# Kernel optimization log

Measured on AMD Instinct MI355X. Metric: run time of the kernel, lower is better.

## Reference

```python
import jax, jax.numpy as jnp
import numpy as np

HIDDEN = 1024
HEADS = 16
HEAD_DIM = HIDDEN // HEADS

def setup_inputs() -> dict:
    key = jax.random.key(0)
    k1, k2, k3 = jax.random.split(key, 3)
    scale = 1.0 / np.sqrt(HIDDEN)
    return {
        "x": jax.random.normal(k1, (2, 2048, HIDDEN), dtype=jnp.float32),
        "w_qkv": jax.random.normal(k2, (HIDDEN, 3 * HIDDEN), dtype=jnp.float32) * scale,
        "b_qkv": jnp.zeros((3 * HIDDEN,), dtype=jnp.float32),
        "w_out": jax.random.normal(k3, (HIDDEN, HIDDEN), dtype=jnp.float32) * scale,
        "b_out": jnp.zeros((HIDDEN,), dtype=jnp.float32),
    }

def reference(x, w_qkv, b_qkv, w_out, b_out):
    B, S, H = x.shape
    qkv = x @ w_qkv + b_qkv                              # (B,S,3H)
    qkv = qkv.reshape(B, S, 3, HEADS, HEAD_DIM)
    qkv = jnp.transpose(qkv, (2, 0, 3, 1, 4))            # (3,B,nh,S,hd)
    q, k, v = qkv[0], qkv[1], qkv[2]
    scores = jnp.einsum("bhqd,bhkd->bhqk", q, k) / np.sqrt(HEAD_DIM)
    causal = jnp.triu(jnp.ones((S, S), dtype=bool), k=1)  # True above diagonal
    scores = jnp.where(causal, -jnp.inf, scores)
    attn = jax.nn.softmax(scores, axis=-1)               # dropout: eval mode (identity)
    out = jnp.einsum("bhqk,bhkd->bhqd", attn, v)
    out = jnp.transpose(out, (0, 2, 1, 3)).reshape(B, S, H)
    return out @ w_out + b_out
```

## Files before the change

kernel.cpp:

```cpp
#include <hip/hip_runtime.h>
#include <hip/hip_bf16.h>

typedef short short8 __attribute__((ext_vector_type(8)));
typedef short short4v __attribute__((ext_vector_type(4)));
typedef unsigned int uint4v __attribute__((ext_vector_type(4)));
typedef float f32x4 __attribute__((ext_vector_type(4)));

typedef const __attribute__((address_space(1))) unsigned int* gas_ptr;
typedef __attribute__((address_space(3))) unsigned int* las_ptr;
#define ASYNC16(g, l) __builtin_amdgcn_global_load_lds((gas_ptr)(g), (las_ptr)(l), 16, 0, 0)

__device__ __forceinline__ unsigned short f2bf(float f) {
    unsigned int u = __builtin_bit_cast(unsigned int, f);
    u += 0x7fff + ((u >> 16) & 1);
    return (unsigned short)(u >> 16);
}
__device__ __forceinline__ float bf2f(unsigned short s) {
    unsigned int u = (unsigned int)s << 16;
    return __builtin_bit_cast(float, u);
}
__device__ __forceinline__ unsigned int pkbf_trunc(float lo, float hi) {
    return __builtin_amdgcn_perm(__builtin_bit_cast(unsigned int, hi),
                                 __builtin_bit_cast(unsigned int, lo), 0x07060302u);
}

__device__ __forceinline__ void transpose_tile(
    const float* __restrict__ w, unsigned short* __restrict__ wt,
    int K, int N, int k0, int n0, unsigned short* tile)
{
    for (int i = threadIdx.x; i < 64 * 64; i += 256) {
        int r = i >> 6, c = i & 63;
        tile[r * 65 + c] = f2bf(w[(size_t)(k0 + r) * N + n0 + c]);
    }
    __syncthreads();
    for (int i = threadIdx.x; i < 64 * 64; i += 256) {
        int r = i >> 6, c = i & 63;
        wt[(size_t)(n0 + r) * K + k0 + c] = tile[c * 65 + r];
    }
}

__global__ __launch_bounds__(256) void prep(
    const float* __restrict__ x, const float* __restrict__ w_qkv,
    const float* __restrict__ w_out,
    unsigned short* __restrict__ x_b, unsigned short* __restrict__ wqkv_t,
    unsigned short* __restrict__ wout_t)
{
    __shared__ unsigned short tile[64 * 65];
    int bid = blockIdx.x;
    if (bid < 4096) {
        int i = (bid * 256 + threadIdx.x) * 4;
        float4 v = *(const float4*)(x + i);
        ushort4 o;
        o.x = f2bf(v.x); o.y = f2bf(v.y); o.z = f2bf(v.z); o.w = f2bf(v.w);
        *(ushort4*)(x_b + i) = o;
    } else if (bid < 4096 + 768) {
        int t = bid - 4096;
        transpose_tile(w_qkv, wqkv_t, 1024, 3072, (t / 48) * 64, (t % 48) * 64, tile);
    } else {
        int t = bid - 4864;
        transpose_tile(w_out, wout_t, 1024, 1024, (t >> 4) * 64, (t & 15) * 64, tile);
    }
}


template<bool OUT_BF16, bool QKV>
__global__ __launch_bounds__(256, 3) void gemm_bt(
    const unsigned short* __restrict__ A,
    const unsigned short* __restrict__ Bt,
    const float* __restrict__ bias,
    void* __restrict__ C,
    unsigned short* __restrict__ vTp,
    int M, int N, int K)
{
    __shared__ __align__(16) unsigned short As[128 * 32];
    __shared__ __align__(16) unsigned short Bs[128 * 32];
    const int tid = threadIdx.x;
    const int lane = tid & 63;
    const int wave = tid >> 6;
    const int wr = wave >> 1, wc = wave & 1;
    const int m0 = blockIdx.x * 128, n0 = blockIdx.y * 128;
    const int fr = lane & 15, fq = lane >> 4;

    f32x4 acc[4][4] = {};

    const int grow = lane >> 2;
    const int gcol = (lane & 3) * 8;
    const unsigned short* Ag = A  + (size_t)(m0 + wave * 32 + grow) * K + gcol;
    const unsigned short* Bg = Bt + (size_t)(n0 + wave * 32 + grow) * K + gcol;
    unsigned short* AsW0 = As + (wave * 32) * 32;
    unsigned short* AsW1 = As + (wave * 32 + 16) * 32;
    unsigned short* BsW0 = Bs + (wave * 32) * 32;
    unsigned short* BsW1 = Bs + (wave * 32 + 16) * 32;

    for (int k0 = 0; k0 < K; k0 += 32) {
        __syncthreads();
        ASYNC16(Ag + k0,          AsW0);
        ASYNC16(Ag + 16 * K + k0, AsW1);
        ASYNC16(Bg + k0,          BsW0);
        ASYNC16(Bg + 16 * K + k0, BsW1);
        __syncthreads();

        short8 af[4], bfr[4];
#pragma unroll
        for (int i = 0; i < 4; i++)
            af[i] = *(const short8*)(As + (wr * 64 + i * 16 + fr) * 32 + fq * 8);
#pragma unroll
        for (int j = 0; j < 4; j++)
            bfr[j] = *(const short8*)(Bs + (wc * 64 + j * 16 + fr) * 32 + fq * 8);
#pragma unroll
        for (int i = 0; i < 4; i++)
#pragma unroll
            for (int j = 0; j < 4; j++)
                acc[i][j] = __builtin_amdgcn_mfma_f32_16x16x32_bf16(af[i], bfr[j], acc[i][j], 0, 0, 0);
    }

#pragma unroll
    for (int i = 0; i < 4; i++)
#pragma unroll
        for (int j = 0; j < 4; j++) {
            int col = n0 + wc * 64 + j * 16 + fr;
            float bv = bias[col];
            if (QKV && col >= 2048) {
                int hh = (col - 2048) >> 6, d = col & 63;
#pragma unroll
                for (int r = 0; r < 4; r++) {
                    int row = m0 + wr * 64 + i * 16 + fq * 4 + r;
                    int bb = row >> 11, s = row & 2047;
                    vTp[((size_t)(bb * 16 + hh) * 64 + d) * 2048 + s] = f2bf(acc[i][j][r] + bv);
                }
            } else {
                const int cstride = QKV ? 2048 : N;
#pragma unroll
                for (int r = 0; r < 4; r++) {
                    int row = m0 + wr * 64 + i * 16 + fq * 4 + r;
                    float v = acc[i][j][r] + bv;
                    if (OUT_BF16)
                        ((unsigned short*)C)[(size_t)row * cstride + col] = f2bf(v);
                    else
                        ((float*)C)[(size_t)row * cstride + col] = v;
                }
            }
        }
}


template<int RG0>
__device__ __forceinline__ void attn_step(
    const unsigned short* __restrict__ Ks0, const unsigned short* __restrict__ Ks1,
    const unsigned short* __restrict__ Vs0, const unsigned short* __restrict__ Vs1,
    const short8 (&qf)[4][2], const short8 ones,
    f32x4 (&o_acc)[4][4], f32x4 (&l_acc)[4],
    int j0, int fr, int fq,
    const int (&qrow0)[4], bool diagA, bool diagB)
{
    short8 kf[4][2];
#pragma unroll
    for (int t = 0; t < 4; t++) {
        kf[t][0] = *(const short8*)(Ks0 + (t * 16 + fr) * 32 + fq * 8);
        kf[t][1] = *(const short8*)(Ks1 + (t * 16 + fr) * 32 + fq * 8);
    }

    short8 pf[4][2];
#pragma unroll
    for (int rg = RG0; rg < 4; rg++) {
        f32x4 s[4];
#pragma unroll
        for (int t = 0; t < 4; t++) {
            s[t] = (f32x4){0.f, 0.f, 0.f, 0.f};
            s[t] = __builtin_amdgcn_mfma_f32_16x16x32_bf16(kf[t][0], qf[rg][0], s[t], 0, 0, 0);
            s[t] = __builtin_amdgcn_mfma_f32_16x16x32_bf16(kf[t][1], qf[rg][1], s[t], 0, 0, 0);
        }
        const bool diag = (rg < 2) ? diagA : diagB;
        unsigned int pk[4][2];
        if (diag) {
            const int qq = qrow0[rg] + fr;
#pragma unroll
            for (int t = 0; t < 4; t++) {
                const int keyb = j0 + t * 16 + fq * 4;
                float p[4];
#pragma unroll
                for (int r = 0; r < 4; r++) {
                    float v = __expf(s[t][r] * 0.125f - 8.0f);
                    if (keyb + r > qq) v = 0.f;
                    p[r] = v;
                }
                pk[t][0] = pkbf_trunc(p[0], p[1]);
                pk[t][1] = pkbf_trunc(p[2], p[3]);
            }
        } else {
#pragma unroll
            for (int t = 0; t < 4; t++) {
                float p[4];
#pragma unroll
                for (int r = 0; r < 4; r++)
                    p[r] = __expf(s[t][r] * 0.125f - 8.0f);
                pk[t][0] = pkbf_trunc(p[0], p[1]);
                pk[t][1] = pkbf_trunc(p[2], p[3]);
            }
        }
        pf[rg][0] = __builtin_bit_cast(short8, (uint4v){pk[0][0], pk[0][1], pk[1][0], pk[1][1]});
        pf[rg][1] = __builtin_bit_cast(short8, (uint4v){pk[2][0], pk[2][1], pk[3][0], pk[3][1]});
    }

#pragma unroll
    for (int ks = 0; ks < 2; ks++) {
        const unsigned short* Vsb = ks ? Vs1 : Vs0;
#pragma unroll
        for (int t = 0; t < 4; t++) {
            short4v vlo = *(const short4v*)(Vsb + (t * 16 + fr) * 32 + fq * 4);
            short4v vhi = *(const short4v*)(Vsb + (t * 16 + fr) * 32 + 16 + fq * 4);
            short8 vf = (short8){vlo[0], vlo[1], vlo[2], vlo[3], vhi[0], vhi[1], vhi[2], vhi[3]};
#pragma unroll
            for (int rg = RG0; rg < 4; rg++)
                o_acc[rg][t] = __builtin_amdgcn_mfma_f32_16x16x32_bf16(vf, pf[rg][ks], o_acc[rg][t], 0, 0, 0);
        }
#pragma unroll
        for (int rg = RG0; rg < 4; rg++)
            l_acc[rg] = __builtin_amdgcn_mfma_f32_16x16x32_bf16(ones, pf[rg][ks], l_acc[rg], 0, 0, 0);
    }
}

__global__ __launch_bounds__(128, 2) void flash_attn(
    const unsigned short* __restrict__ qkv,
    const unsigned short* __restrict__ vT,
    unsigned short* __restrict__ Opart,
    float* __restrict__ lpart)
{
    const int gid = blockIdx.x;
    const int bh = gid & 31;
    const int sl = gid >> 5;
    const int p  = sl & 15;
    const int g  = sl >> 4;
    const int h = bh & 15, b = bh >> 4;
    const int tid = threadIdx.x, wave = tid >> 6, lane = tid & 63;
    const int fr = lane & 15, fq = lane >> 4;
    const size_t RS = 2048;

    const unsigned short* Qb = qkv + (size_t)b * 2048 * RS + h * 64;
    const unsigned short* Kb = Qb + 1024;
    const unsigned short* Vt = vT + (size_t)(b * 16 + h) * 64 * 2048;

    __shared__ __align__(16) unsigned short Ks[2][64 * 32];
    __shared__ __align__(16) unsigned short Vs[2][64 * 32];

    short8 qf[4][2];
    int qrow0[4];
#pragma unroll
    for (int rg = 0; rg < 4; rg++) {
        int qt = (rg < 2) ? p : (31 - p);
        qrow0[rg] = qt * 64 + wave * 32 + (rg & 1) * 16;
        const unsigned short* qrow = Qb + (size_t)(qrow0[rg] + fr) * RS;
        qf[rg][0] = *(const short8*)(qrow + fq * 8);
        qf[rg][1] = *(const short8*)(qrow + 32 + fq * 8);
    }
    short8 ones;
#pragma unroll
    for (int e = 0; e < 8; e++) ones[e] = (short)0x3F80;

    f32x4 o_acc[4][4] = {};
    f32x4 l_acc[4] = {};

    const int grow = lane >> 2;
    const int gcol = (lane & 3) * 8;
    const unsigned short* Kg = Kb + (size_t)(wave * 32 + grow) * RS + gcol;
    const unsigned short* Vg = Vt + (size_t)(wave * 32 + grow) * 2048 + gcol;
    unsigned short* KsW00 = Ks[0] + (wave * 32) * 32;
    unsigned short* KsW01 = Ks[0] + (wave * 32 + 16) * 32;
    unsigned short* KsW10 = Ks[1] + (wave * 32) * 32;
    unsigned short* KsW11 = Ks[1] + (wave * 32 + 16) * 32;
    unsigned short* VsW00 = Vs[0] + (wave * 32) * 32;
    unsigned short* VsW01 = Vs[0] + (wave * 32 + 16) * 32;
    unsigned short* VsW10 = Vs[1] + (wave * 32) * 32;
    unsigned short* VsW11 = Vs[1] + (wave * 32 + 16) * 32;

    const int njt = 32 - p;
    int lo = (g == 0) ? 0 : njt;
    int hi = njt;
    {
        int cum = 0;
        bool flo = (g == 0), fhi = false;
        for (int j = 0; j < njt; j++) {
            if (!flo && cum >= 44 * g)        { lo = j; flo = true; }
            if (!fhi && cum >= 44 * (g + 1))  { hi = j; fhi = true; }
            cum += (j <= p) ? 8 : 4;
        }
    }

    for (int jt = lo; jt < hi; jt++) {
        const int j0 = jt * 64;
        __syncthreads();
        ASYNC16(Kg + (size_t)j0 * RS,               KsW00);
        ASYNC16(Kg + (size_t)(j0 + 16) * RS,        KsW01);
        ASYNC16(Kg + (size_t)j0 * RS + 32,          KsW10);
        ASYNC16(Kg + (size_t)(j0 + 16) * RS + 32,   KsW11);
        ASYNC16(Vg + j0,               VsW00);
        ASYNC16(Vg + 16 * 2048 + j0,   VsW01);
        ASYNC16(Vg + j0 + 32,          VsW10);
        ASYNC16(Vg + 16 * 2048 + j0 + 32, VsW11);
        __syncthreads();

        bool diagA = (jt == p), diagB = (jt == 31 - p);
        if (jt <= p)
            attn_step<0>(Ks[0], Ks[1], Vs[0], Vs[1], qf, ones,
                         o_acc, l_acc, j0, fr, fq, qrow0, diagA, diagB);
        else
            attn_step<2>(Ks[0], Ks[1], Vs[0], Vs[1], qf, ones,
                         o_acc, l_acc, j0, fr, fq, qrow0, diagA, diagB);
    }

    unsigned short* Og = Opart + (size_t)g * 4096 * 1024;
    float* lg = lpart + (size_t)g * 4096 * 16;
#pragma unroll
    for (int rg = 0; rg < 4; rg++) {
        const size_t rowbase = (size_t)(b * 2048 + qrow0[rg] + fr) * 1024 + h * 64;
#pragma unroll
        for (int t = 0; t < 4; t++) {
            ushort4 o;
            o.x = f2bf(o_acc[rg][t][0]); o.y = f2bf(o_acc[rg][t][1]);
            o.z = f2bf(o_acc[rg][t][2]); o.w = f2bf(o_acc[rg][t][3]);
            *(ushort4*)(Og + rowbase + t * 16 + fq * 4) = o;
        }
        if (fq == 0)
            lg[(size_t)(b * 2048 + qrow0[rg] + fr) * 16 + h] = l_acc[rg][0];
    }
}

__global__ __launch_bounds__(256) void reduce_attn(
    const unsigned short* __restrict__ Opart, const float* __restrict__ lpart,
    unsigned short* __restrict__ out)
{
    const size_t OP = (size_t)4096 * 1024, LP = (size_t)4096 * 16;
    int i = (blockIdx.x * 256 + threadIdx.x) * 8;
    int row = i >> 10, h = (i & 1023) >> 6;
    float lsum = lpart[row * 16 + h] + lpart[LP + row * 16 + h] + lpart[2 * LP + row * 16 + h];
    float inv = 1.0f / lsum;
    float acc[8];
#pragma unroll
    for (int e = 0; e < 8; e++) acc[e] = 0.f;
#pragma unroll
    for (int gpart = 0; gpart < 3; gpart++) {
        ushort4 a0 = *(const ushort4*)(Opart + gpart * OP + i);
        ushort4 a1 = *(const ushort4*)(Opart + gpart * OP + i + 4);
        acc[0] += bf2f(a0.x); acc[1] += bf2f(a0.y); acc[2] += bf2f(a0.z); acc[3] += bf2f(a0.w);
        acc[4] += bf2f(a1.x); acc[5] += bf2f(a1.y); acc[6] += bf2f(a1.z); acc[7] += bf2f(a1.w);
    }
    ushort4 o0, o1;
    o0.x = f2bf(acc[0] * inv); o0.y = f2bf(acc[1] * inv);
    o0.z = f2bf(acc[2] * inv); o0.w = f2bf(acc[3] * inv);
    o1.x = f2bf(acc[4] * inv); o1.y = f2bf(acc[5] * inv);
    o1.z = f2bf(acc[6] * inv); o1.w = f2bf(acc[7] * inv);
    *(ushort4*)(out + i) = o0;
    *(ushort4*)(out + i + 4) = o1;
}

extern "C" void kernel_launch(void* const* d_in, const int* in_sizes, int n_in,
                              void* d_out, int out_size, void* d_ws, size_t ws_size,
                              hipStream_t stream) {
    const float* x      = (const float*)d_in[0];
    const float* w_qkv  = (const float*)d_in[1];
    const float* b_qkv  = (const float*)d_in[2];
    const float* w_out  = (const float*)d_in[3];
    const float* b_out  = (const float*)d_in[4];
    float* out = (float*)d_out;

    char* ws = (char*)d_ws;
    const size_t MB = 1024 * 1024;
    unsigned short* qkv    = (unsigned short*)(ws);
    unsigned short* vT     = (unsigned short*)(ws + 16 * MB);
    unsigned short* wout_t = (unsigned short*)(ws + 24 * MB);
    unsigned short* attn   = (unsigned short*)(ws + 26 * MB);
    float*          lpart  = (float*)         (ws + 34 * MB);
    unsigned short* x_b    = (unsigned short*)(ws + 36 * MB);
    unsigned short* wqkv_t = (unsigned short*)(ws + 44 * MB);
    unsigned short* Opart  = (unsigned short*)(ws + 36 * MB);

    prep<<<5120, 256, 0, stream>>>(x, w_qkv, w_out, x_b, wqkv_t, wout_t);
    gemm_bt<true, true ><<<dim3(32, 24), 256, 0, stream>>>(x_b,  wqkv_t, b_qkv, qkv, vT, 4096, 3072, 1024);
    flash_attn<<<1536, 128, 0, stream>>>(qkv, vT, Opart, lpart);
    reduce_attn<<<2048, 256, 0, stream>>>(Opart, lpart, attn);
    gemm_bt<false, false><<<dim3(32, 8),  256, 0, stream>>>(attn, wout_t, b_out, out, nullptr, 4096, 1024, 1024);
}
```

Measured before the change: 212.0 us.

## Rework flash attention to 4 waves per block with 2-way KV split

Flash attention blocks now run four waves of 16 query rows each instead of two waves of 32. The key range is split into two partitions with a simple fixed midpoint instead of three partitions balanced by a cost loop, and the reduce kernel sums two partials instead of three. The V tile is now written to LDS with a per-row rotation and read back with the matching offset, to cut bank conflicts on the V fragment loads. Each wave holds fewer accumulators, which should allow more resident waves, but the fixed split may balance work unevenly across blocks.

```diff
diff --git a/kernel.cpp b/kernel.cpp
--- a/kernel.cpp
+++ b/kernel.cpp
@@ -148,10 +148,10 @@
 __device__ __forceinline__ void attn_step(
     const unsigned short* __restrict__ Ks0, const unsigned short* __restrict__ Ks1,
     const unsigned short* __restrict__ Vs0, const unsigned short* __restrict__ Vs1,
-    const short8 (&qf)[4][2], const short8 ones,
-    f32x4 (&o_acc)[4][4], f32x4 (&l_acc)[4],
+    const short8 (&qf)[2][2], const short8 ones,
+    f32x4 (&o_acc)[2][4], f32x4 (&l_acc)[2],
     int j0, int fr, int fq,
-    const int (&qrow0)[4], bool diagA, bool diagB)
+    const int (&qrow0)[2], bool diagA, bool diagB)
 {
     short8 kf[4][2];
 #pragma unroll
@@ -160,9 +160,9 @@
         kf[t][1] = *(const short8*)(Ks1 + (t * 16 + fr) * 32 + fq * 8);
     }
 
-    short8 pf[4][2];
-#pragma unroll
-    for (int rg = RG0; rg < 4; rg++) {
+    short8 pf[2][2];
+#pragma unroll
+    for (int rg = RG0; rg < 2; rg++) {
         f32x4 s[4];
 #pragma unroll
         for (int t = 0; t < 4; t++) {
@@ -170,7 +170,7 @@
             s[t] = __builtin_amdgcn_mfma_f32_16x16x32_bf16(kf[t][0], qf[rg][0], s[t], 0, 0, 0);
             s[t] = __builtin_amdgcn_mfma_f32_16x16x32_bf16(kf[t][1], qf[rg][1], s[t], 0, 0, 0);
         }
-        const bool diag = (rg < 2) ? diagA : diagB;
+        const bool diag = rg ? diagB : diagA;
         unsigned int pk[4][2];
         if (diag) {
             const int qq = qrow0[rg] + fr;
@@ -202,25 +202,28 @@
         pf[rg][1] = __builtin_bit_cast(short8, (uint4v){pk[2][0], pk[2][1], pk[3][0], pk[3][1]});
     }
 
+    const int rot = (fr & 3) * 8;
+    const int eo_lo = (fq * 4 - rot) & 31;
+    const int eo_hi = (fq * 4 + 16 - rot) & 31;
 #pragma unroll
     for (int ks = 0; ks < 2; ks++) {
         const unsigned short* Vsb = ks ? Vs1 : Vs0;
 #pragma unroll
         for (int t = 0; t < 4; t++) {
-            short4v vlo = *(const short4v*)(Vsb + (t * 16 + fr) * 32 + fq * 4);
-            short4v vhi = *(const short4v*)(Vsb + (t * 16 + fr) * 32 + 16 + fq * 4);
+            short4v vlo = *(const short4v*)(Vsb + (t * 16 + fr) * 32 + eo_lo);
+            short4v vhi = *(const short4v*)(Vsb + (t * 16 + fr) * 32 + eo_hi);
             short8 vf = (short8){vlo[0], vlo[1], vlo[2], vlo[3], vhi[0], vhi[1], vhi[2], vhi[3]};
 #pragma unroll
-            for (int rg = RG0; rg < 4; rg++)
+            for (int rg = RG0; rg < 2; rg++)
                 o_acc[rg][t] = __builtin_amdgcn_mfma_f32_16x16x32_bf16(vf, pf[rg][ks], o_acc[rg][t], 0, 0, 0);
         }
 #pragma unroll
-        for (int rg = RG0; rg < 4; rg++)
+        for (int rg = RG0; rg < 2; rg++)
             l_acc[rg] = __builtin_amdgcn_mfma_f32_16x16x32_bf16(ones, pf[rg][ks], l_acc[rg], 0, 0, 0);
     }
 }
 
-__global__ __launch_bounds__(128, 2) void flash_attn(
+__global__ __launch_bounds__(256, 3) void flash_attn(
     const unsigned short* __restrict__ qkv,
     const unsigned short* __restrict__ vT,
     unsigned short* __restrict__ Opart,
@@ -243,12 +246,12 @@
     __shared__ __align__(16) unsigned short Ks[2][64 * 32];
     __shared__ __align__(16) unsigned short Vs[2][64 * 32];
 
-    short8 qf[4][2];
-    int qrow0[4];
-#pragma unroll
-    for (int rg = 0; rg < 4; rg++) {
-        int qt = (rg < 2) ? p : (31 - p);
-        qrow0[rg] = qt * 64 + wave * 32 + (rg & 1) * 16;
+    short8 qf[2][2];
+    int qrow0[2];
+#pragma unroll
+    for (int rg = 0; rg < 2; rg++) {
+        int qt = rg ? (31 - p) : p;
+        qrow0[rg] = qt * 64 + wave * 16;
         const unsigned short* qrow = Qb + (size_t)(qrow0[rg] + fr) * RS;
         qf[rg][0] = *(const short8*)(qrow + fq * 8);
         qf[rg][1] = *(const short8*)(qrow + 32 + fq * 8);
@@ -257,46 +260,31 @@
 #pragma unroll
     for (int e = 0; e < 8; e++) ones[e] = (short)0x3F80;
 
-    f32x4 o_acc[4][4] = {};
-    f32x4 l_acc[4] = {};
+    f32x4 o_acc[2][4] = {};
+    f32x4 l_acc[2] = {};
 
     const int grow = lane >> 2;
     const int gcol = (lane & 3) * 8;
-    const unsigned short* Kg = Kb + (size_t)(wave * 32 + grow) * RS + gcol;
-    const unsigned short* Vg = Vt + (size_t)(wave * 32 + grow) * 2048 + gcol;
-    unsigned short* KsW00 = Ks[0] + (wave * 32) * 32;
-    unsigned short* KsW01 = Ks[0] + (wave * 32 + 16) * 32;
-    unsigned short* KsW10 = Ks[1] + (wave * 32) * 32;
-    unsigned short* KsW11 = Ks[1] + (wave * 32 + 16) * 32;
-    unsigned short* VsW00 = Vs[0] + (wave * 32) * 32;
-    unsigned short* VsW01 = Vs[0] + (wave * 32 + 16) * 32;
-    unsigned short* VsW10 = Vs[1] + (wave * 32) * 32;
-    unsigned short* VsW11 = Vs[1] + (wave * 32 + 16) * 32;
-
-    const int njt = 32 - p;
-    int lo = (g == 0) ? 0 : njt;
-    int hi = njt;
-    {
-        int cum = 0;
-        bool flo = (g == 0), fhi = false;
-        for (int j = 0; j < njt; j++) {
-            if (!flo && cum >= 44 * g)        { lo = j; flo = true; }
-            if (!fhi && cum >= 44 * (g + 1))  { hi = j; fhi = true; }
-            cum += (j <= p) ? 8 : 4;
-        }
-    }
+    const int vrot = (grow & 3) * 8;
+    const int vcol = (gcol + vrot) & 31;
+    const unsigned short* Kg = Kb + (size_t)(wave * 16 + grow) * RS + gcol;
+    const unsigned short* Vg = Vt + (size_t)(wave * 16 + grow) * 2048 + vcol;
+    unsigned short* KsW0 = Ks[0] + (wave * 16) * 32;
+    unsigned short* KsW1 = Ks[1] + (wave * 16) * 32;
+    unsigned short* VsW0 = Vs[0] + (wave * 16) * 32;
+    unsigned short* VsW1 = Vs[1] + (wave * 16) * 32;
+
+    const int mid = (p >= 8) ? 8 : (16 - p);
+    const int lo = g ? mid : 0;
+    const int hi = g ? (32 - p) : mid;
 
     for (int jt = lo; jt < hi; jt++) {
         const int j0 = jt * 64;
         __syncthreads();
-        ASYNC16(Kg + (size_t)j0 * RS,               KsW00);
-        ASYNC16(Kg + (size_t)(j0 + 16) * RS,        KsW01);
-        ASYNC16(Kg + (size_t)j0 * RS + 32,          KsW10);
-        ASYNC16(Kg + (size_t)(j0 + 16) * RS + 32,   KsW11);
-        ASYNC16(Vg + j0,               VsW00);
-        ASYNC16(Vg + 16 * 2048 + j0,   VsW01);
-        ASYNC16(Vg + j0 + 32,          VsW10);
-        ASYNC16(Vg + 16 * 2048 + j0 + 32, VsW11);
+        ASYNC16(Kg + (size_t)j0 * RS,      KsW0);
+        ASYNC16(Kg + (size_t)j0 * RS + 32, KsW1);
+        ASYNC16(Vg + j0,      VsW0);
+        ASYNC16(Vg + j0 + 32, VsW1);
         __syncthreads();
 
         bool diagA = (jt == p), diagB = (jt == 31 - p);
@@ -304,14 +292,14 @@
             attn_step<0>(Ks[0], Ks[1], Vs[0], Vs[1], qf, ones,
                          o_acc, l_acc, j0, fr, fq, qrow0, diagA, diagB);
         else
-            attn_step<2>(Ks[0], Ks[1], Vs[0], Vs[1], qf, ones,
+            attn_step<1>(Ks[0], Ks[1], Vs[0], Vs[1], qf, ones,
                          o_acc, l_acc, j0, fr, fq, qrow0, diagA, diagB);
     }
 
     unsigned short* Og = Opart + (size_t)g * 4096 * 1024;
     float* lg = lpart + (size_t)g * 4096 * 16;
 #pragma unroll
-    for (int rg = 0; rg < 4; rg++) {
+    for (int rg = 0; rg < 2; rg++) {
         const size_t rowbase = (size_t)(b * 2048 + qrow0[rg] + fr) * 1024 + h * 64;
 #pragma unroll
         for (int t = 0; t < 4; t++) {
@@ -332,23 +320,21 @@
     const size_t OP = (size_t)4096 * 1024, LP = (size_t)4096 * 16;
     int i = (blockIdx.x * 256 + threadIdx.x) * 8;
     int row = i >> 10, h = (i & 1023) >> 6;
-    float lsum = lpart[row * 16 + h] + lpart[LP + row * 16 + h] + lpart[2 * LP + row * 16 + h];
+    float lsum = lpart[row * 16 + h] + lpart[LP + row * 16 + h];
     float inv = 1.0f / lsum;
-    float acc[8];
-#pragma unroll
-    for (int e = 0; e < 8; e++) acc[e] = 0.f;
-#pragma unroll
-    for (int gpart = 0; gpart < 3; gpart++) {
-        ushort4 a0 = *(const ushort4*)(Opart + gpart * OP + i);
-        ushort4 a1 = *(const ushort4*)(Opart + gpart * OP + i + 4);
-        acc[0] += bf2f(a0.x); acc[1] += bf2f(a0.y); acc[2] += bf2f(a0.z); acc[3] += bf2f(a0.w);
-        acc[4] += bf2f(a1.x); acc[5] += bf2f(a1.y); acc[6] += bf2f(a1.z); acc[7] += bf2f(a1.w);
-    }
+    ushort4 a0 = *(const ushort4*)(Opart + i);
+    ushort4 a1 = *(const ushort4*)(Opart + i + 4);
+    ushort4 b0 = *(const ushort4*)(Opart + OP + i);
+    ushort4 b1 = *(const ushort4*)(Opart + OP + i + 4);
     ushort4 o0, o1;
-    o0.x = f2bf(acc[0] * inv); o0.y = f2bf(acc[1] * inv);
-    o0.z = f2bf(acc[2] * inv); o0.w = f2bf(acc[3] * inv);
-    o1.x = f2bf(acc[4] * inv); o1.y = f2bf(acc[5] * inv);
-    o1.z = f2bf(acc[6] * inv); o1.w = f2bf(acc[7] * inv);
+    o0.x = f2bf((bf2f(a0.x) + bf2f(b0.x)) * inv);
+    o0.y = f2bf((bf2f(a0.y) + bf2f(b0.y)) * inv);
+    o0.z = f2bf((bf2f(a0.z) + bf2f(b0.z)) * inv);
+    o0.w = f2bf((bf2f(a0.w) + bf2f(b0.w)) * inv);
+    o1.x = f2bf((bf2f(a1.x) + bf2f(b1.x)) * inv);
+    o1.y = f2bf((bf2f(a1.y) + bf2f(b1.y)) * inv);
+    o1.z = f2bf((bf2f(a1.z) + bf2f(b1.z)) * inv);
+    o1.w = f2bf((bf2f(a1.w) + bf2f(b1.w)) * inv);
     *(ushort4*)(out + i) = o0;
     *(ushort4*)(out + i + 4) = o1;
 }
@@ -376,7 +362,7 @@
 
     prep<<<5120, 256, 0, stream>>>(x, w_qkv, w_out, x_b, wqkv_t, wout_t);
     gemm_bt<true, true ><<<dim3(32, 24), 256, 0, stream>>>(x_b,  wqkv_t, b_qkv, qkv, vT, 4096, 3072, 1024);
-    flash_attn<<<1536, 128, 0, stream>>>(qkv, vT, Opart, lpart);
+    flash_attn<<<1024, 256, 0, stream>>>(qkv, vT, Opart, lpart);
     reduce_attn<<<2048, 256, 0, stream>>>(Opart, lpart, attn);
     gemm_bt<false, false><<<dim3(32, 8),  256, 0, stream>>>(attn, wout_t, b_out, out, nullptr, 4096, 1024, 1024);
 }
```

Result: faster. 194.2 us (-8.4%).
